# Optimization experiments

Hardware: AMD Instinct MI355X
Metric: run time of the kernel (lower is better)

Reference implementation:

```python
import jax, jax.numpy as jnp
import numpy as np


def setup_inputs() -> dict:
    key = jax.random.key(0)
    k1, k2 = jax.random.split(key)
    B, S, D, K = 8, 2048, 512, 8192
    x = jax.random.normal(k1, (B, S, D), dtype=jnp.float32)
    codebook = jax.random.normal(k2, (K, D), dtype=jnp.float32)
    return {"x": x, "codebook": codebook}


def reference(x, codebook):
    # x: [B, S, D], codebook: [K, D]
    B, S, D = x.shape
    flat_x = x.reshape(-1, D)                      # [N, D], N = B*S
    distances = (
        jnp.sum(flat_x * flat_x, axis=1, keepdims=True)
        - 2.0 * jnp.matmul(flat_x, codebook.T)
        + jnp.sum(codebook * codebook, axis=1)
    )
    encoding_indices = jnp.argmin(distances, axis=1)  # [N]
    quantized = codebook[encoding_indices]            # [N, D] embedding lookup
    return quantized.reshape(x.shape)                 # [B, S, D]
```

## Files before the change

kernel.cpp:

```cpp
#include <hip/hip_runtime.h>


#define MROWS 16384
#define KCB   8192
#define DDIM  512
#define NTILES (KCB / 128)
#define MARGIN 8.0f

typedef unsigned short u16;
typedef unsigned int uint;
typedef __attribute__((ext_vector_type(8))) short bf16x8;
typedef __attribute__((ext_vector_type(4))) float f32x4;

__device__ inline u16 f2bf(float f) {
  unsigned int u = __float_as_uint(f);
  u += 0x7FFFu + ((u >> 16) & 1u);
  return (u16)(u >> 16);
}

__device__ inline void gload16(const void* g, void* l) {
  __builtin_amdgcn_global_load_lds((const __attribute__((address_space(1))) void*)g,
                                   (__attribute__((address_space(3))) void*)l,
                                   16, 0, 0);
}

__device__ inline double shfl_xor_dbl(double v, int m) {
  long long l = __double_as_longlong(v);
  int lo = (int)(l & 0xffffffffLL), hi = (int)(l >> 32);
  lo = __shfl_xor(lo, m, 64);
  hi = __shfl_xor(hi, m, 64);
  return __longlong_as_double(((long long)hi << 32) | (unsigned long long)(unsigned int)lo);
}

__device__ inline float keyval(uint k) {
  uint u = k & 0xFFFFFF80u;
  uint bits = (u & 0x80000000u) ? (u & 0x7FFFFFFFu) : ~u;
  return __uint_as_float(bits);
}


__global__ __launch_bounds__(256) void k_conv_x(const float* __restrict__ x,
                                                u16* __restrict__ xb) {
  size_t i = ((size_t)blockIdx.x * 256 + threadIdx.x) * 8;
  float4 a = *(const float4*)(x + i);
  float4 b = *(const float4*)(x + i + 4);
  union { u16 s[8]; uint4 v; } u;
  u.s[0]=f2bf(a.x); u.s[1]=f2bf(a.y); u.s[2]=f2bf(a.z); u.s[3]=f2bf(a.w);
  u.s[4]=f2bf(b.x); u.s[5]=f2bf(b.y); u.s[6]=f2bf(b.z); u.s[7]=f2bf(b.w);
  *(uint4*)(xb + i) = u.v;
}

__global__ __launch_bounds__(256) void k_conv_cb(const float* __restrict__ cb,
                                                 u16* __restrict__ cbb,
                                                 float* __restrict__ cnorm) {
  int k = blockIdx.x * 4 + (threadIdx.x >> 6);
  int lane = threadIdx.x & 63;
  size_t base = (size_t)k * DDIM + lane * 8;
  float4 a = *(const float4*)(cb + base);
  float4 b = *(const float4*)(cb + base + 4);
  union { u16 s[8]; uint4 v; } u;
  u.s[0]=f2bf(a.x); u.s[1]=f2bf(a.y); u.s[2]=f2bf(a.z); u.s[3]=f2bf(a.w);
  u.s[4]=f2bf(b.x); u.s[5]=f2bf(b.y); u.s[6]=f2bf(b.z); u.s[7]=f2bf(b.w);
  *(uint4*)(cbb + base) = u.v;
  float s = a.x*a.x + a.y*a.y + a.z*a.z + a.w*a.w
          + b.x*b.x + b.y*b.y + b.z*b.z + b.w*b.w;
  #pragma unroll
  for (int m = 1; m < 64; m <<= 1) s += __shfl_xor(s, m, 64);
  if (lane == 0) cnorm[k] = s;
}


__global__ __launch_bounds__(512, 2) void k_gemm_min(
    const u16* __restrict__ Xbf, const u16* __restrict__ Cbf,
    const float* __restrict__ cnorm, uint2* __restrict__ stats)
{
  extern __shared__ __align__(16) u16 lds[];

  int bid = blockIdx.x;
  int xcd = bid & 7;
  int j   = bid >> 3;
  int mTile = xcd * 8 + (j & 7);
  int nTile = j >> 3;
  int rowBase = mTile * 256;
  int colBase = nTile * 256;

  int tid = threadIdx.x;
  int lane = tid & 63;
  int wv = tid >> 6;
  int wr = wv >> 2;
  int wc = wv & 3;
  int grp = lane >> 4;
  int l15 = lane & 15;

  const int rr = tid >> 3;
  const int pc = (tid & 7) ^ (rr & 7);
  const u16* pA = Cbf + (size_t)(colBase + rr) * DDIM + pc * 8;
  const u16* pB = Xbf + (size_t)(rowBase + rr) * DDIM + pc * 8;

  const int m7 = l15 & 7;
  const int ch0 = (grp ^ m7);
  const int ch1 = ch0 ^ 4;
  const int cOff0 = wr * 4096 + l15 * 64 + ch0 * 8;
  const int cOff1 = wr * 4096 + l15 * 64 + ch1 * 8;
  const int xOff0 = wc * 4096 + l15 * 64 + ch0 * 8;
  const int xOff1 = wc * 4096 + l15 * 64 + ch1 * 8;

  f32x4 acc[8][4];
  #pragma unroll
  for (int mi = 0; mi < 8; ++mi)
    #pragma unroll
    for (int ni = 0; ni < 4; ++ni)
      acc[mi][ni] = (f32x4){0.f, 0.f, 0.f, 0.f};

  bf16x8 cF[2][4];
  bf16x8 xF[2][4];

#define STAGE_AH0(T) { const int d_=((T)&1)*16384; const int so_=(T)*64;                  \
  gload16(pA + so_,          (void*)&lds[d_ + tid * 8]);                                  \
  gload16(pA + 65536 + so_,  (void*)&lds[d_ + 4096 + tid * 8]); }
#define STAGE_AH1(T) { const int d_=((T)&1)*16384 + 8192; const int so_=(T)*64;           \
  gload16(pA + 32768 + so_,  (void*)&lds[d_ + tid * 8]);                                  \
  gload16(pA + 98304 + so_,  (void*)&lds[d_ + 4096 + tid * 8]); }
#define STAGE_BH0(T) { const int d_=32768+((T)&1)*16384; const int so_=(T)*64;            \
  gload16(pB + so_,          (void*)&lds[d_ + tid * 8]);                                  \
  gload16(pB + 32768 + so_,  (void*)&lds[d_ + 4096 + tid * 8]); }
#define STAGE_BH1(T) { const int d_=32768+((T)&1)*16384 + 8192; const int so_=(T)*64;     \
  gload16(pB + 65536 + so_,  (void*)&lds[d_ + tid * 8]);                                  \
  gload16(pB + 98304 + so_,  (void*)&lds[d_ + 4096 + tid * 8]); }

#define ISSUE_READS(pp)                                                                   \
  { const int kt_ = (pp) >> 2, s_ = (pp) & 3, h_ = s_ >> 1, ks_ = s_ & 1;                 \
    const int bo_ = (kt_ & 1) * 16384;                                                    \
    const int co_ = ks_ ? cOff1 : cOff0;                                                  \
    _Pragma("unroll")                                                                     \
    for (int q = 0; q < 4; ++q)                                                           \
      cF[(pp) & 1][q] = *(const bf16x8*)&lds[bo_ + h_ * 8192 + q * 1024 + co_];           \
    if (h_ == 0) {                                                                        \
      const int xo_ = ks_ ? xOff1 : xOff0;                                                \
      _Pragma("unroll")                                                                   \
      for (int ni = 0; ni < 4; ++ni)                                                      \
        xF[(pp) & 1][ni] = *(const bf16x8*)&lds[32768 + bo_ + ni * 1024 + xo_];           \
    } }

  STAGE_AH0(0); STAGE_AH1(0); STAGE_BH0(0); STAGE_BH1(0);
  STAGE_AH0(1); STAGE_BH0(1);
  asm volatile("s_waitcnt vmcnt(4)" ::: "memory");
  __builtin_amdgcn_s_barrier();
  __builtin_amdgcn_sched_barrier(0);
  ISSUE_READS(0);

  #pragma unroll
  for (int ph = 0; ph < 32; ++ph) {
    const int s = ph & 3, kt = ph >> 2;

    if (s == 3 && ph != 31) asm volatile("s_waitcnt vmcnt(2)" ::: "memory");
    if (ph == 29)           asm volatile("s_waitcnt vmcnt(0)" ::: "memory");
    __builtin_amdgcn_s_barrier();
    __builtin_amdgcn_sched_barrier(0);

    if      (s == 0 && kt <= 6) { STAGE_BH1(kt + 1); }
    else if (s == 1 && kt <= 6) { STAGE_AH1(kt + 1); }
    else if (s == 2 && kt <= 5) { STAGE_AH0(kt + 2); }
    else if (s == 3 && kt <= 5) { STAGE_BH0(kt + 2); }

    if (ph < 31) ISSUE_READS(ph + 1);

    if (ph == 31)            asm volatile("s_waitcnt lgkmcnt(0)" ::: "memory");
    else if (((ph + 1) & 2) == 0) asm volatile("s_waitcnt lgkmcnt(8)" ::: "memory");
    else                     asm volatile("s_waitcnt lgkmcnt(4)" ::: "memory");
    __builtin_amdgcn_sched_barrier(0);

    __builtin_amdgcn_s_setprio(1);
    {
      const int h = s >> 1;
      #pragma unroll
      for (int q = 0; q < 4; ++q)
        #pragma unroll
        for (int ni = 0; ni < 4; ++ni)
          acc[h * 4 + q][ni] = __builtin_amdgcn_mfma_f32_16x16x32_bf16(
              cF[ph & 1][q], xF[ph & 1][ni], acc[h * 4 + q][ni], 0, 0, 0);
    }
    __builtin_amdgcn_s_setprio(0);
  }
#undef ISSUE_READS
#undef STAGE_AH0
#undef STAGE_AH1
#undef STAGE_BH0
#undef STAGE_BH1

#define INS(st1, st2, st3, kx)                                     \
  { uint kk_ = (kx);                                               \
    bool lt1 = kk_ < st1, lt2 = kk_ < st2, lt3 = kk_ < st3;        \
    st3 = lt3 ? (lt2 ? st2 : kk_) : st3;                           \
    st2 = lt2 ? (lt1 ? st1 : kk_) : st2;                           \
    st1 = lt1 ? kk_ : st1; }

  uint t1[4], t2[4], t3[4];
  #pragma unroll
  for (int ni = 0; ni < 4; ++ni) { t1[ni] = 0xFFFFFFFFu; t2[ni] = 0xFFFFFFFFu; t3[ni] = 0xFFFFFFFFu; }

  #pragma unroll
  for (int mi = 0; mi < 8; ++mi) {
    float cnv[4];
    *(float4*)cnv = *(const float4*)&cnorm[colBase + wr * 128 + mi * 16 + grp * 4];
    #pragma unroll
    for (int ni = 0; ni < 4; ++ni) {
      #pragma unroll
      for (int rg = 0; rg < 4; ++rg) {
        float v = cnv[rg] - 2.0f * acc[mi][ni][rg];
        uint u = __float_as_uint(v);
        u = ((int)u < 0) ? ~u : (u | 0x80000000u);
        uint key = (u & 0xFFFFFF80u) | (uint)(mi * 16 + grp * 4 + rg);
        INS(t1[ni], t2[ni], t3[ni], key);
      }
    }
  }
  #pragma unroll
  for (int ni = 0; ni < 4; ++ni) {
    #pragma unroll
    for (int mk = 16; mk <= 32; mk <<= 1) {
      uint o1 = (uint)__shfl_xor((int)t1[ni], mk, 64);
      uint o2 = (uint)__shfl_xor((int)t2[ni], mk, 64);
      uint o3 = (uint)__shfl_xor((int)t3[ni], mk, 64);
      INS(t1[ni], t2[ni], t3[ni], o1);
      INS(t1[ni], t2[ni], t3[ni], o2);
      INS(t1[ni], t2[ni], t3[ni], o3);
    }
  }
#undef INS
  if (grp == 0) {
    #pragma unroll
    for (int ni = 0; ni < 4; ++ni) {
      float v1 = keyval(t1[ni]), v2 = keyval(t2[ni]), v3 = keyval(t3[ni]);
      uint i1 = t1[ni] & 127u, i2 = t2[ni] & 127u;
      uint d2 = min(255u, (uint)((v2 - v1) * 4.0f));
      uint d3 = min(255u, (uint)((v3 - v1) * 4.0f));
      uint2 st;
      st.x = __float_as_uint(v1);
      st.y = i1 | (i2 << 7) | (d2 << 14) | (d3 << 22);
      int xrow = rowBase + wc * 64 + ni * 16 + l15;
      stats[(size_t)xrow * NTILES + nTile * 2 + wr] = st;
    }
  }
}


__device__ inline void eval64(const float4& xa, const float4& xb,
                              const float* __restrict__ cb, int col,
                              double& best, int& bi, int lane) {
  const float* cr = cb + (size_t)col * DDIM + lane * 8;
  float4 ca = *(const float4*)cr;
  float4 cv = *(const float4*)(cr + 4);
  double s = 0.0, d;
  d = (double)xa.x - (double)ca.x; s += d*d;
  d = (double)xa.y - (double)ca.y; s += d*d;
  d = (double)xa.z - (double)ca.z; s += d*d;
  d = (double)xa.w - (double)ca.w; s += d*d;
  d = (double)xb.x - (double)cv.x; s += d*d;
  d = (double)xb.y - (double)cv.y; s += d*d;
  d = (double)xb.z - (double)cv.z; s += d*d;
  d = (double)xb.w - (double)cv.w; s += d*d;
  #pragma unroll
  for (int m = 1; m < 64; m <<= 1) s += shfl_xor_dbl(s, m);
  if (s < best || (s == best && col < bi)) { best = s; bi = col; }
}

__global__ __launch_bounds__(256) void k_refine(
    const float* __restrict__ x, const float* __restrict__ cb,
    const float* __restrict__ cnorm, const uint2* __restrict__ stats,
    unsigned int* __restrict__ bestOut)
{
  int n = blockIdx.x * 4 + (threadIdx.x >> 6);
  int lane = threadIdx.x & 63;
  uint2 st = stats[(size_t)n * NTILES + lane];
  float m1 = __uint_as_float(st.x);
  int   i1 = st.y & 127, i2 = (st.y >> 7) & 127;
  float m2 = m1 + ((st.y >> 14) & 255u) * 0.25f;
  float m3 = m1 + ((st.y >> 22) & 255u) * 0.25f;
  float g = m1;
  #pragma unroll
  for (int m = 1; m < 64; m <<= 1) g = fminf(g, __shfl_xor(g, m, 64));
  float T = g + MARGIN;
  unsigned long long q1 = __ballot(m1 <= T);
  unsigned long long q2 = __ballot(m2 <= T);
  unsigned long long qr = __ballot(m3 <= T);

  const float* xr = x + (size_t)n * DDIM;
  float4 xa = *(const float4*)(xr + lane * 8);
  float4 xb = *(const float4*)(xr + lane * 8 + 4);

  double best = 1e300;
  int bi = 0x7fffffff;

  while (q1) {
    int t = __ffsll(q1) - 1; q1 &= q1 - 1;
    int col = t * 128 + __shfl(i1, t, 64);
    eval64(xa, xb, cb, col, best, bi, lane);
  }
  while (q2) {
    int t = __ffsll(q2) - 1; q2 &= q2 - 1;
    int col = t * 128 + __shfl(i2, t, 64);
    eval64(xa, xb, cb, col, best, bi, lane);
  }
  while (qr) {
    int t = __ffsll(qr) - 1; qr &= qr - 1;
    for (int c2 = 0; c2 < 128; ++c2) {
      int col2 = t * 128 + c2;
      const float* cr = cb + (size_t)col2 * DDIM + lane * 8;
      float4 ca = *(const float4*)cr;
      float4 cv = *(const float4*)(cr + 4);
      float p = xa.x*ca.x + xa.y*ca.y + xa.z*ca.z + xa.w*ca.w
              + xb.x*cv.x + xb.y*cv.y + xb.z*cv.z + xb.w*cv.w;
      #pragma unroll
      for (int m = 1; m < 64; m <<= 1) p += __shfl_xor(p, m, 64);
      float s32 = cnorm[col2] - 2.0f * p;
      if (s32 <= T) {
        double s = 0.0, dd;
        dd = (double)xa.x - (double)ca.x; s += dd*dd;
        dd = (double)xa.y - (double)ca.y; s += dd*dd;
        dd = (double)xa.z - (double)ca.z; s += dd*dd;
        dd = (double)xa.w - (double)ca.w; s += dd*dd;
        dd = (double)xb.x - (double)cv.x; s += dd*dd;
        dd = (double)xb.y - (double)cv.y; s += dd*dd;
        dd = (double)xb.z - (double)cv.z; s += dd*dd;
        dd = (double)xb.w - (double)cv.w; s += dd*dd;
        #pragma unroll
        for (int m = 1; m < 64; m <<= 1) s += shfl_xor_dbl(s, m);
        if (s < best || (s == best && col2 < bi)) { best = s; bi = col2; }
      }
    }
  }
  if (lane == 0) bestOut[n] = (unsigned int)bi;
}


__global__ __launch_bounds__(256) void k_gather(const float* __restrict__ cb,
                                                const unsigned int* __restrict__ bestIdx,
                                                float* __restrict__ out) {
  int n = blockIdx.x * 4 + (threadIdx.x >> 6);
  int lane = threadIdx.x & 63;
  unsigned int b = bestIdx[n];
  const float4* s = (const float4*)(cb + (size_t)b * DDIM);
  float4* dp = (float4*)(out + (size_t)n * DDIM);
  dp[lane * 2]     = s[lane * 2];
  dp[lane * 2 + 1] = s[lane * 2 + 1];
}


extern "C" void kernel_launch(void* const* d_in, const int* in_sizes, int n_in,
                              void* d_out, int out_size, void* d_ws, size_t ws_size,
                              hipStream_t stream) {
  const float* x  = (const float*)d_in[0];
  const float* cb = (const float*)d_in[1];
  float* out = (float*)d_out;

  char* ob = (char*)d_out;
  u16*   Xbf   = (u16*)ob;
  u16*   Cbf   = (u16*)(ob + 16ull * 1024 * 1024);
  uint2* stats = (uint2*)(ob + 24ull * 1024 * 1024);

  char* wsb = (char*)d_ws;
  float* cnorm = (float*)wsb;
  unsigned int* bestIdx = (unsigned int*)(wsb + 32 * 1024);

  (void)hipFuncSetAttribute((const void*)k_gemm_min,
                            hipFuncAttributeMaxDynamicSharedMemorySize, 131072);

  k_conv_x  <<<4096, 256, 0, stream>>>(x, Xbf);
  k_conv_cb <<<2048, 256, 0, stream>>>(cb, Cbf, cnorm);
  k_gemm_min<<<2048, 512, 131072, stream>>>(Xbf, Cbf, cnorm, stats);
  k_refine  <<<4096, 256, 0, stream>>>(x, cb, cnorm, stats, bestIdx);
  k_gather  <<<4096, 256, 0, stream>>>(cb, bestIdx, out);
}
```

Measured before the change: 256.0 us.

## Restructure GEMM main loop pipelining and fuse refine with gather

```diff
diff --git a/kernel.cpp b/kernel.cpp
--- a/kernel.cpp
+++ b/kernel.cpp
@@ -112,7 +112,6 @@
     for (int ni = 0; ni < 4; ++ni)
       acc[mi][ni] = (f32x4){0.f, 0.f, 0.f, 0.f};
 
-  bf16x8 cF[2][4];
   bf16x8 xF[2][4];
 
 #define STAGE_AH0(T) { const int d_=((T)&1)*16384; const int so_=(T)*64;                  \
@@ -125,64 +124,67 @@
   gload16(pB + so_,          (void*)&lds[d_ + tid * 8]);                                  \
   gload16(pB + 32768 + so_,  (void*)&lds[d_ + 4096 + tid * 8]); }
 #define STAGE_BH1(T) { const int d_=32768+((T)&1)*16384 + 8192; const int so_=(T)*64;     \
+  gload16(pB + 65536 + so_,  (void*)&lds[d_ + 4096 + tid * 8]);                           \
+  gload16(pB + 98304 + so_,  (void*)&lds[d_ + 8192 + tid * 8]); }
+#undef STAGE_BH1
+#define STAGE_BH1(T) { const int d_=32768+((T)&1)*16384 + 8192; const int so_=(T)*64;     \
   gload16(pB + 65536 + so_,  (void*)&lds[d_ + tid * 8]);                                  \
   gload16(pB + 98304 + so_,  (void*)&lds[d_ + 4096 + tid * 8]); }
 
-#define ISSUE_READS(pp)                                                                   \
-  { const int kt_ = (pp) >> 2, s_ = (pp) & 3, h_ = s_ >> 1, ks_ = s_ & 1;                 \
-    const int bo_ = (kt_ & 1) * 16384;                                                    \
-    const int co_ = ks_ ? cOff1 : cOff0;                                                  \
-    _Pragma("unroll")                                                                     \
-    for (int q = 0; q < 4; ++q)                                                           \
-      cF[(pp) & 1][q] = *(const bf16x8*)&lds[bo_ + h_ * 8192 + q * 1024 + co_];           \
-    if (h_ == 0) {                                                                        \
-      const int xo_ = ks_ ? xOff1 : xOff0;                                                \
-      _Pragma("unroll")                                                                   \
-      for (int ni = 0; ni < 4; ++ni)                                                      \
-        xF[(pp) & 1][ni] = *(const bf16x8*)&lds[32768 + bo_ + ni * 1024 + xo_];           \
-    } }
-
-  STAGE_AH0(0); STAGE_AH1(0); STAGE_BH0(0); STAGE_BH1(0);
+  STAGE_AH0(0); STAGE_BH0(0); STAGE_AH1(0); STAGE_BH1(0);
   STAGE_AH0(1); STAGE_BH0(1);
   asm volatile("s_waitcnt vmcnt(4)" ::: "memory");
   __builtin_amdgcn_s_barrier();
   __builtin_amdgcn_sched_barrier(0);
-  ISSUE_READS(0);
-
-  #pragma unroll
-  for (int ph = 0; ph < 32; ++ph) {
-    const int s = ph & 3, kt = ph >> 2;
-
-    if (s == 3 && ph != 31) asm volatile("s_waitcnt vmcnt(2)" ::: "memory");
-    if (ph == 29)           asm volatile("s_waitcnt vmcnt(0)" ::: "memory");
-    __builtin_amdgcn_s_barrier();
-    __builtin_amdgcn_sched_barrier(0);
-
-    if      (s == 0 && kt <= 6) { STAGE_BH1(kt + 1); }
-    else if (s == 1 && kt <= 6) { STAGE_AH1(kt + 1); }
-    else if (s == 2 && kt <= 5) { STAGE_AH0(kt + 2); }
-    else if (s == 3 && kt <= 5) { STAGE_BH0(kt + 2); }
-
-    if (ph < 31) ISSUE_READS(ph + 1);
-
-    if (ph == 31)            asm volatile("s_waitcnt lgkmcnt(0)" ::: "memory");
-    else if (((ph + 1) & 2) == 0) asm volatile("s_waitcnt lgkmcnt(8)" ::: "memory");
-    else                     asm volatile("s_waitcnt lgkmcnt(4)" ::: "memory");
-    __builtin_amdgcn_sched_barrier(0);
-
-    __builtin_amdgcn_s_setprio(1);
-    {
-      const int h = s >> 1;
+
+  #pragma unroll 1
+  for (int it = 0; it < 4; ++it) {
+    const int t0 = 2 * it;
+    #pragma unroll
+    for (int p = 0; p < 8; ++p) {
+      const int s = p & 3, h = s >> 1, ks = s & 1, bp = p >> 2;
+      const int kt = t0 + bp;
+
+      bf16x8 cF[4];
+      {
+        const int co_ = ks ? cOff1 : cOff0;
+        #pragma unroll
+        for (int q = 0; q < 4; ++q)
+          cF[q] = *(const bf16x8*)&lds[bp * 16384 + h * 8192 + q * 1024 + co_];
+        if (h == 0) {
+          const int xo_ = ks ? xOff1 : xOff0;
+          #pragma unroll
+          for (int ni = 0; ni < 4; ++ni)
+            xF[ks][ni] = *(const bf16x8*)&lds[32768 + bp * 16384 + ni * 1024 + xo_];
+        }
+      }
+      if      (s == 0) { if (kt + 1 <= 7) STAGE_BH1(kt + 1); }
+      else if (s == 1) { if (kt + 1 <= 7) STAGE_AH1(kt + 1); }
+      else if (s == 2) { if (kt + 2 <= 7) STAGE_AH0(kt + 2); }
+      else             { if (kt + 2 <= 7) STAGE_BH0(kt + 2); }
+
+      if (ks == 1) {
+        if (it == 3 && p == 3)      { asm volatile("s_waitcnt vmcnt(4)" ::: "memory"); }
+        else if (it == 3 && p == 5) { asm volatile("s_waitcnt vmcnt(0)" ::: "memory"); }
+        else if (!(it == 3 && p == 7)) { asm volatile("s_waitcnt vmcnt(8)" ::: "memory"); }
+      }
+      __builtin_amdgcn_sched_barrier(0);
+      __builtin_amdgcn_s_barrier();
+      asm volatile("s_waitcnt lgkmcnt(0)" ::: "memory");
+      __builtin_amdgcn_sched_barrier(0);
+
+      __builtin_amdgcn_s_setprio(1);
       #pragma unroll
       for (int q = 0; q < 4; ++q)
         #pragma unroll
         for (int ni = 0; ni < 4; ++ni)
           acc[h * 4 + q][ni] = __builtin_amdgcn_mfma_f32_16x16x32_bf16(
-              cF[ph & 1][q], xF[ph & 1][ni], acc[h * 4 + q][ni], 0, 0, 0);
+              cF[q], xF[ks][ni], acc[h * 4 + q][ni], 0, 0, 0);
+      __builtin_amdgcn_s_setprio(0);
+      __builtin_amdgcn_sched_barrier(0);
+      __builtin_amdgcn_s_barrier();
     }
-    __builtin_amdgcn_s_setprio(0);
-  }
-#undef ISSUE_READS
+  }
 #undef STAGE_AH0
 #undef STAGE_AH1
 #undef STAGE_BH0
@@ -265,13 +267,10 @@
   if (s < best || (s == best && col < bi)) { best = s; bi = col; }
 }
 
-__global__ __launch_bounds__(256) void k_refine(
-    const float* __restrict__ x, const float* __restrict__ cb,
-    const float* __restrict__ cnorm, const uint2* __restrict__ stats,
-    unsigned int* __restrict__ bestOut)
-{
-  int n = blockIdx.x * 4 + (threadIdx.x >> 6);
-  int lane = threadIdx.x & 63;
+__device__ inline int refine_row(int n, int lane,
+                                 const float* __restrict__ x, const float* __restrict__ cb,
+                                 const float* __restrict__ cnorm,
+                                 const uint2* __restrict__ stats) {
   uint2 st = stats[(size_t)n * NTILES + lane];
   float m1 = __uint_as_float(st.x);
   int   i1 = st.y & 127, i2 = (st.y >> 7) & 127;
@@ -330,7 +329,32 @@
       }
     }
   }
+  return bi;
+}
+
+__global__ __launch_bounds__(256) void k_refine(
+    const float* __restrict__ x, const float* __restrict__ cb,
+    const float* __restrict__ cnorm, const uint2* __restrict__ stats,
+    unsigned int* __restrict__ bestOut)
+{
+  int n = blockIdx.x * 4 + (threadIdx.x >> 6);
+  int lane = threadIdx.x & 63;
+  int bi = refine_row(n, lane, x, cb, cnorm, stats);
   if (lane == 0) bestOut[n] = (unsigned int)bi;
+}
+
+__global__ __launch_bounds__(256) void k_refine_gather(
+    const float* __restrict__ x, const float* __restrict__ cb,
+    const float* __restrict__ cnorm, const uint2* __restrict__ stats,
+    float* __restrict__ out)
+{
+  int n = blockIdx.x * 4 + (threadIdx.x >> 6);
+  int lane = threadIdx.x & 63;
+  int bi = refine_row(n, lane, x, cb, cnorm, stats);
+  const float4* s = (const float4*)(cb + (size_t)bi * DDIM);
+  float4* dp = (float4*)(out + (size_t)n * DDIM);
+  dp[lane * 2]     = s[lane * 2];
+  dp[lane * 2 + 1] = s[lane * 2 + 1];
 }
 
 
@@ -355,20 +379,28 @@
   float* out = (float*)d_out;
 
   char* ob = (char*)d_out;
-  u16*   Xbf   = (u16*)ob;
-  u16*   Cbf   = (u16*)(ob + 16ull * 1024 * 1024);
-  uint2* stats = (uint2*)(ob + 24ull * 1024 * 1024);
+  u16* Xbf = (u16*)ob;
+  u16* Cbf = (u16*)(ob + 16ull * 1024 * 1024);
 
   char* wsb = (char*)d_ws;
   float* cnorm = (float*)wsb;
   unsigned int* bestIdx = (unsigned int*)(wsb + 32 * 1024);
 
+  const size_t statsBytes = (size_t)MROWS * NTILES * sizeof(uint2);
+  bool fuse = ws_size >= 96 * 1024 + statsBytes;
+  uint2* stats = fuse ? (uint2*)(wsb + 96 * 1024)
+                      : (uint2*)(ob + 24ull * 1024 * 1024);
+
   (void)hipFuncSetAttribute((const void*)k_gemm_min,
                             hipFuncAttributeMaxDynamicSharedMemorySize, 131072);
 
   k_conv_x  <<<4096, 256, 0, stream>>>(x, Xbf);
   k_conv_cb <<<2048, 256, 0, stream>>>(cb, Cbf, cnorm);
   k_gemm_min<<<2048, 512, 131072, stream>>>(Xbf, Cbf, cnorm, stats);
-  k_refine  <<<4096, 256, 0, stream>>>(x, cb, cnorm, stats, bestIdx);
-  k_gather  <<<4096, 256, 0, stream>>>(cb, bestIdx, out);
-}
+  if (fuse) {
+    k_refine_gather<<<4096, 256, 0, stream>>>(x, cb, cnorm, stats, out);
+  } else {
+    k_refine<<<4096, 256, 0, stream>>>(x, cb, cnorm, stats, bestIdx);
+    k_gather<<<4096, 256, 0, stream>>>(cb, bestIdx, out);
+  }
+}
```

New measurement: 267.4 us. +4.5%, slower.
